# Kernel tuning notes

Measured on AMD Instinct MI355X. Metric: run time of the kernel, lower is better.

## Reference

```python
import jax, jax.numpy as jnp
import numpy as np

TOTAL = 131072   # total frames across all utterances
SEG = 256        # number of utterances
FEAT = 78        # input feature dim (hardcoded by Linear(78,1024))
HID = 1024
NCLS = 10


def _linear_params(key, fan_in, fan_out):
    # torch nn.Linear default init: U(-1/sqrt(fan_in), 1/sqrt(fan_in))
    bound = 1.0 / np.sqrt(fan_in)
    kw, kb = jax.random.split(key)
    W = jax.random.uniform(kw, (fan_in, fan_out), minval=-bound, maxval=bound, dtype=jnp.float32)
    b = jax.random.uniform(kb, (fan_out,), minval=-bound, maxval=bound, dtype=jnp.float32)
    return W, b


def setup_inputs() -> dict:
    key = jax.random.key(0)
    ks = jax.random.split(key, 8)
    # ragged lengths summing exactly to TOTAL
    rng = np.random.default_rng(0)
    raw = rng.integers(256, 768, size=SEG).astype(np.float64)
    lens = np.maximum(1, (raw * TOTAL / raw.sum()).astype(np.int64))
    lens[-1] += TOTAL - lens.sum()
    lengths = jnp.asarray(lens, dtype=jnp.int32)

    x = jax.random.normal(ks[0], (TOTAL, FEAT), dtype=jnp.float32)
    W1, b1 = _linear_params(ks[1], FEAT, HID)
    W2, b2 = _linear_params(ks[2], HID, HID)
    W3, b3 = _linear_params(ks[3], HID, HID)
    W4, b4 = _linear_params(ks[4], HID, HID)
    W5, b5 = _linear_params(ks[5], HID, 1)
    W6, b6 = _linear_params(ks[6], HID, HID)
    W7, b7 = _linear_params(ks[7], HID, NCLS)
    return dict(x=x, W1=W1, b1=b1, W2=W2, b2=b2, W3=W3, b3=b3, W4=W4, b4=b4,
                W5=W5, b5=b5, W6=W6, b6=b6, W7=W7, b7=b7, lengths=lengths)


def reference(x, W1, b1, W2, b2, W3, b3, W4, b4, W5, b5, W6, b6, W7, b7, lengths):
    h = jax.nn.relu(x @ W1 + b1)
    h = jax.nn.relu(h @ W2 + b2)
    h = jax.nn.relu(h @ W3 + b3)
    h = jax.nn.relu(h @ W4 + b4)            # [N, HID]
    scores = jax.nn.relu(h @ W5 + b5)[:, 0]  # per-frame attention logit [N]

    # per-segment softmax over frames, then weighted sum pooling (fused segment ops)
    n_seg = lengths.shape[0]
    seg = jnp.repeat(jnp.arange(n_seg, dtype=jnp.int32), lengths,
                     total_repeat_length=h.shape[0])          # [N] segment ids
    m = jax.ops.segment_max(scores, seg, num_segments=n_seg)  # stable softmax max
    e = jnp.exp(scores - m[seg])
    denom = jax.ops.segment_sum(e, seg, num_segments=n_seg)
    w = e / denom[seg]                                        # [N] softmax weights
    pooled = jax.ops.segment_sum(h * w[:, None], seg, num_segments=n_seg)  # [SEG, HID]

    out = jax.nn.relu(pooled @ W6 + b6) @ W7 + b7             # [SEG, 10]
    return out
```

## Files before the change

### kernel.cpp

```cpp
#include <hip/hip_runtime.h>
#include <hip/hip_fp16.h>

#define TOTAL 131072
#define SEGN  256
#define FEAT  78
#define FPAD  96
#define HID   1024
#define NCLS  10
#define FCHUNK 32

typedef __attribute__((ext_vector_type(8))) short short8;
typedef __attribute__((ext_vector_type(4))) float floatx4;

typedef __attribute__((address_space(1))) void gvoid_t;
typedef __attribute__((address_space(3))) void svoid_t;

__device__ __forceinline__ void async_copy16(const void* gsrc, void* ldst) {
    __builtin_amdgcn_global_load_lds((gvoid_t*)(void*)gsrc, (svoid_t*)ldst, 16, 0, 0);
}


__global__ void conv_x_slab(const float* __restrict__ x, __half* __restrict__ xb,
                            int row0, int rows) {
    int idx = blockIdx.x * 256 + threadIdx.x;
    if (idx >= rows * FPAD) return;
    int col = idx % FPAD;
    int r   = idx / FPAD;
    float v = (col < FEAT) ? x[(size_t)(row0 + r) * FEAT + col] : 0.0f;
    xb[idx] = __float2half(v);
}

__global__ void conv_wt_kernel(const float* __restrict__ W, __half* __restrict__ Wt,
                               int K, int N, int Kpad) {
    int idx = blockIdx.x * 256 + threadIdx.x;
    if (idx >= N * Kpad) return;
    int k = idx % Kpad;
    int n = idx / Kpad;
    float v = (k < K) ? W[(size_t)k * N + n] : 0.0f;
    Wt[idx] = __float2half(v);
}

__global__ void conv_w4_kernel(const float* __restrict__ W2, const float* __restrict__ W3,
                               const float* __restrict__ W4, const float* __restrict__ W6,
                               __half* __restrict__ w2t, __half* __restrict__ w3t,
                               __half* __restrict__ w4t, __half* __restrict__ w6t) {
    int idx = blockIdx.x * 256 + threadIdx.x;
    if (idx >= HID * HID) return;
    int k = idx % HID;
    int n = idx / HID;
    const float* Ws[4] = {W2, W3, W4, W6};
    __half* Ts[4] = {w2t, w3t, w4t, w6t};
    int w = blockIdx.y;
    Ts[w][idx] = __float2half(Ws[w][(size_t)k * HID + n]);
}


#define VMCNT(n)  asm volatile("s_waitcnt vmcnt(" #n ")" ::: "memory")
#define SBAR      __builtin_amdgcn_s_barrier()

#define STAGE_A(TT) do { short* d_ = smem + (((TT)&3)<<14); \
    async_copy16(gA + (TT)*32, d_ + t*8); \
    async_copy16(gA + (TT)*32 + kstr128, d_ + 4096 + t*8); } while (0)
#define STAGE_B(TT) do { short* d_ = smem + (((TT)&3)<<14) + 8192; \
    async_copy16(gB + (TT)*32, d_ + t*8); \
    async_copy16(gB + (TT)*32 + kstr128, d_ + 4096 + t*8); } while (0)

#define TILE_BODY(TT, DO_STAGE, VM) do { \
    const short* base_ = smem + (((TT)&3)<<14); \
    short8 af0_[4], af1_[4], bf_[4]; \
    _Pragma("unroll") \
    for (int i_ = 0; i_ < 4; ++i_) af0_[i_] = *(const short8*)&base_[aoff + i_*512]; \
    _Pragma("unroll") \
    for (int i_ = 0; i_ < 4; ++i_) bf_[i_]  = *(const short8*)&base_[8192 + boff + i_*512]; \
    _Pragma("unroll") \
    for (int i_ = 0; i_ < 4; ++i_) af1_[i_] = *(const short8*)&base_[2048 + aoff + i_*512]; \
    if (DO_STAGE) { STAGE_A((TT)+3); STAGE_B((TT)+3); } \
    __builtin_amdgcn_s_setprio(1); \
    _Pragma("unroll") \
    for (int mi_ = 0; mi_ < 4; ++mi_) \
        _Pragma("unroll") \
        for (int ni_ = 0; ni_ < 4; ++ni_) \
            acc[mi_][ni_] = __builtin_amdgcn_mfma_f32_16x16x32_f16( \
                af0_[mi_], bf_[ni_], acc[mi_][ni_], 0, 0, 0); \
    _Pragma("unroll") \
    for (int mi_ = 0; mi_ < 4; ++mi_) \
        _Pragma("unroll") \
        for (int ni_ = 0; ni_ < 4; ++ni_) \
            acc[4+mi_][ni_] = __builtin_amdgcn_mfma_f32_16x16x32_f16( \
                af1_[mi_], bf_[ni_], acc[4+mi_][ni_], 0, 0, 0); \
    __builtin_amdgcn_s_setprio(0); \
    VM; \
    SBAR; \
} while (0)

__global__ __launch_bounds__(512, 2)
void gemm256(const __half* __restrict__ A, const __half* __restrict__ Bt,
             __half* __restrict__ C, const float* __restrict__ bias,
             int M, int N, int K, int relu_flag,
             const float* __restrict__ W5g, float* __restrict__ scores_p)
{
    __shared__ __align__(16) short smem[4 * 16384];

    const int t   = threadIdx.x;
    const int nbn = N >> 8;
    const int nbm = M >> 8;
    int bm, bn;
    {
        const int b = blockIdx.x;
        if ((nbm & 7) == 0) {
            const int xcd = b & 7;
            const int j   = b >> 3;
            bm = xcd * (nbm >> 3) + j / nbn;
            bn = j % nbn;
        } else {
            bn = b % nbn;
            bm = b / nbn;
        }
    }
    const size_t m0 = (size_t)bm << 8;
    const size_t n0 = (size_t)bn << 8;
    const int wave = t >> 6, lane = t & 63;
    const int wmb = (wave >> 2) << 7;
    const int wnb = (wave & 3) << 6;
    const int l16 = lane & 15, q = lane >> 4;
    const int qa  = q ^ ((l16 >> 1) & 3);
    const int aoff = (wmb + l16) * 32 + qa * 8;
    const int boff = (wnb + l16) * 32 + qa * 8;

    const int rr = t >> 2;
    const int qs = ((t & 3) ^ ((t >> 3) & 3)) * 8;
    const __half* gA = A  + (m0 + rr) * K + qs;
    const __half* gB = Bt + (n0 + rr) * K + qs;
    const int kstr128 = K << 7;

    floatx4 acc[8][4] = {};
    const int NT = K >> 5;

    STAGE_A(0); STAGE_B(0);
    STAGE_A(1); STAGE_B(1);
    STAGE_A(2); STAGE_B(2);
    VMCNT(4);
    SBAR;

    int T = 0;
    for (; T < NT - 3; ++T)
        TILE_BODY(T, 1, VMCNT(4));
    TILE_BODY(T, 0, VMCNT(0)); ++T;
    TILE_BODY(T, 0, (void)0);  ++T;
    TILE_BODY(T, 0, (void)0);
    __syncthreads();

    __half* ct = (__half*)smem;
#pragma unroll
    for (int ni = 0; ni < 4; ++ni) {
        const int col = wnb + ni * 16 + l16;
        const float bv = bias[n0 + col];
#pragma unroll
        for (int mi = 0; mi < 8; ++mi) {
            const int r0l = wmb + mi * 16 + q * 4;
#pragma unroll
            for (int r = 0; r < 4; ++r) {
                float v = acc[mi][ni][r] + bv;
                if (relu_flag) v = fmaxf(v, 0.0f);
                ct[(r0l + r) * 256 + col] = __float2half(v);
            }
        }
    }
    __syncthreads();
#pragma unroll
    for (int it = 0; it < 16; ++it) {
        const int chunk = it * 512 + t;
        const int row = chunk >> 5;
        const int c32 = chunk & 31;
        short8 v = *(const short8*)&ct[row * 256 + c32 * 8];
        *(short8*)&C[(m0 + row) * N + n0 + c32 * 8] = v;
        if (scores_p) {
            const float* wv = W5g + n0 + c32 * 8;
            float p = 0.f;
#pragma unroll
            for (int j = 0; j < 8; ++j)
                p += __half2float(((const __half*)&v)[j]) * wv[j];
#pragma unroll
            for (int o = 16; o > 0; o >>= 1) p += __shfl_down(p, o, 32);
            if ((t & 31) == 0)
                scores_p[(size_t)bn * M + m0 + row] = p;
        }
    }
}


__global__ __launch_bounds__(256, 2)
void gemm_f16(const __half* __restrict__ A, const __half* __restrict__ Bt,
              __half* __restrict__ C, const float* __restrict__ bias,
              int M, int N, int K, int relu_flag,
              const float* __restrict__ W5g, float* __restrict__ scores_p)
{
    __shared__ __align__(16) short smem[4 * 128 * 32];
    short* lds_a0 = smem;
    short* lds_a1 = smem + 128 * 32;
    short* lds_b0 = smem + 2 * 128 * 32;
    short* lds_b1 = smem + 3 * 128 * 32;

    const int t   = threadIdx.x;
    const int nbn = N >> 7;
    const int nbm = M >> 7;
    int bm, bn;
    {
        const int b = blockIdx.x;
        if ((nbm & 7) == 0) {
            const int xcd = b & 7;
            const int j   = b >> 3;
            bm = xcd * (nbm >> 3) + j / nbn;
            bn = j % nbn;
        } else {
            bn = b % nbn;
            bm = b / nbn;
        }
    }
    const size_t m0 = (size_t)bm * 128;
    const size_t n0 = (size_t)bn * 128;
    const int wave = t >> 6, lane = t & 63;
    const int wm = (wave >> 1) << 6;
    const int wn = (wave & 1) << 6;
    const int l16 = lane & 15, q = lane >> 4;

    floatx4 acc[4][4] = {};

    const int c0 = t, c1 = t + 256;
    const __half* a0 = A  + (m0 + (size_t)(c0 >> 2)) * K + (c0 & 3) * 8;
    const __half* a1 = A  + (m0 + (size_t)(c1 >> 2)) * K + (c1 & 3) * 8;
    const __half* b0 = Bt + (n0 + (size_t)(c0 >> 2)) * K + (c0 & 3) * 8;
    const __half* b1 = Bt + (n0 + (size_t)(c1 >> 2)) * K + (c1 & 3) * 8;
    short* lA0_0 = &lds_a0[c0 * 8];
    short* lA0_1 = &lds_a0[c1 * 8];
    short* lA1_0 = &lds_a1[c0 * 8];
    short* lA1_1 = &lds_a1[c1 * 8];
    short* lB0_0 = &lds_b0[c0 * 8];
    short* lB0_1 = &lds_b0[c1 * 8];
    short* lB1_0 = &lds_b1[c0 * 8];
    short* lB1_1 = &lds_b1[c1 * 8];

    for (int k0 = 0; k0 < K; k0 += 64) {
        __syncthreads();
        async_copy16(a0 + k0, lA0_0);
        async_copy16(a1 + k0, lA0_1);
        async_copy16(b0 + k0, lB0_0);
        async_copy16(b1 + k0, lB0_1);
        async_copy16(a0 + k0 + 32, lA1_0);
        async_copy16(a1 + k0 + 32, lA1_1);
        async_copy16(b0 + k0 + 32, lB1_0);
        async_copy16(b1 + k0 + 32, lB1_1);
        __syncthreads();

        short8 af[4], bfv[4];
#pragma unroll
        for (int i = 0; i < 4; ++i)
            af[i] = *(const short8*)&lds_a0[(wm + i * 16 + l16) * 32 + q * 8];
#pragma unroll
        for (int i = 0; i < 4; ++i)
            bfv[i] = *(const short8*)&lds_b0[(wn + i * 16 + l16) * 32 + q * 8];
#pragma unroll
        for (int mi = 0; mi < 4; ++mi)
#pragma unroll
            for (int ni = 0; ni < 4; ++ni)
                acc[mi][ni] = __builtin_amdgcn_mfma_f32_16x16x32_f16(
                    af[mi], bfv[ni], acc[mi][ni], 0, 0, 0);

#pragma unroll
        for (int i = 0; i < 4; ++i)
            af[i] = *(const short8*)&lds_a1[(wm + i * 16 + l16) * 32 + q * 8];
#pragma unroll
        for (int i = 0; i < 4; ++i)
            bfv[i] = *(const short8*)&lds_b1[(wn + i * 16 + l16) * 32 + q * 8];
#pragma unroll
        for (int mi = 0; mi < 4; ++mi)
#pragma unroll
            for (int ni = 0; ni < 4; ++ni)
                acc[mi][ni] = __builtin_amdgcn_mfma_f32_16x16x32_f16(
                    af[mi], bfv[ni], acc[mi][ni], 0, 0, 0);
    }

    __half* ct = (__half*)smem;
#pragma unroll
    for (int h = 0; h < 2; ++h) {
        __syncthreads();
        if (wm == h * 64) {
#pragma unroll
            for (int ni = 0; ni < 4; ++ni) {
                const int col = wn + ni * 16 + l16;
                const float bv = bias[n0 + col];
#pragma unroll
                for (int mi = 0; mi < 4; ++mi) {
                    const int r0l = mi * 16 + q * 4;
#pragma unroll
                    for (int r = 0; r < 4; ++r) {
                        float v = acc[mi][ni][r] + bv;
                        if (relu_flag) v = fmaxf(v, 0.0f);
                        ct[(r0l + r) * 128 + col] = __float2half(v);
                    }
                }
            }
        }
        __syncthreads();
#pragma unroll
        for (int it = 0; it < 4; ++it) {
            const int chunk = it * 256 + t;
            const int row = chunk >> 4;
            const int off = (chunk & 15) * 8;
            short8 v = *(const short8*)&ct[row * 128 + off];
            *(short8*)&C[(m0 + h * 64 + row) * N + n0 + off] = v;
            if (scores_p) {
                const float* wv = W5g + n0 + off;
                float p = 0.f;
#pragma unroll
                for (int j = 0; j < 8; ++j)
                    p += __half2float(((const __half*)&v)[j]) * wv[j];
#pragma unroll
                for (int o = 8; o > 0; o >>= 1) p += __shfl_down(p, o, 16);
                if (l16 == 0)
                    scores_p[(size_t)bn * M + m0 + h * 64 + row] = p;
            }
        }
    }
}


__global__ __launch_bounds__(256, 2)
void gemm_k96(const __half* __restrict__ A, const __half* __restrict__ Bt,
              __half* __restrict__ C, const float* __restrict__ bias, int M, int N)
{
    __shared__ __align__(16) short smem[2 * 128 * 96];
    short* lds_a = smem;
    short* lds_b = smem + 128 * 96;

    const int t   = threadIdx.x;
    const int nbn = N >> 7;
    const int nbm = M >> 7;
    int bm, bn;
    {
        const int b = blockIdx.x;
        if ((nbm & 7) == 0) {
            const int xcd = b & 7;
            const int j   = b >> 3;
            bm = xcd * (nbm >> 3) + j / nbn;
            bn = j % nbn;
        } else {
            bn = b % nbn;
            bm = b / nbn;
        }
    }
    const size_t m0 = (size_t)bm * 128;
    const size_t n0 = (size_t)bn * 128;
    const int wave = t >> 6, lane = t & 63;
    const int wm = (wave >> 1) << 6;
    const int wn = (wave & 1) << 6;
    const int l16 = lane & 15, q = lane >> 4;

#pragma unroll
    for (int i = 0; i < 6; ++i) {
        const int c = i * 256 + t;
        const int r = c / 12, j = c % 12;
        async_copy16(A  + (m0 + (size_t)r) * 96 + j * 8, &lds_a[c * 8]);
        async_copy16(Bt + (n0 + (size_t)r) * 96 + j * 8, &lds_b[c * 8]);
    }
    __syncthreads();

    floatx4 acc[4][4] = {};
#pragma unroll
    for (int ks = 0; ks < 3; ++ks) {
        short8 af[4], bfv[4];
        const int xo = ks * 32 + q * 8;
#pragma unroll
        for (int i = 0; i < 4; ++i)
            af[i] = *(const short8*)&lds_a[(wm + i * 16 + l16) * 96 + xo];
#pragma unroll
        for (int i = 0; i < 4; ++i)
            bfv[i] = *(const short8*)&lds_b[(wn + i * 16 + l16) * 96 + xo];
#pragma unroll
        for (int mi = 0; mi < 4; ++mi)
#pragma unroll
            for (int ni = 0; ni < 4; ++ni)
                acc[mi][ni] = __builtin_amdgcn_mfma_f32_16x16x32_f16(
                    af[mi], bfv[ni], acc[mi][ni], 0, 0, 0);
    }

    __half* ct = (__half*)smem;
#pragma unroll
    for (int h = 0; h < 2; ++h) {
        __syncthreads();
        if (wm == h * 64) {
#pragma unroll
            for (int ni = 0; ni < 4; ++ni) {
                const int col = wn + ni * 16 + l16;
                const float bv = bias[n0 + col];
#pragma unroll
                for (int mi = 0; mi < 4; ++mi) {
                    const int r0l = mi * 16 + q * 4;
#pragma unroll
                    for (int r = 0; r < 4; ++r) {
                        float v = fmaxf(acc[mi][ni][r] + bv, 0.0f);
                        ct[(r0l + r) * 128 + col] = __float2half(v);
                    }
                }
            }
        }
        __syncthreads();
#pragma unroll
        for (int it = 0; it < 4; ++it) {
            const int chunk = it * 256 + t;
            const int row = chunk >> 4;
            const int off = (chunk & 15) * 8;
            *(short8*)&C[(m0 + h * 64 + row) * N + n0 + off] =
                *(const short8*)&ct[row * 128 + off];
        }
    }
}


__global__ void seg_offsets_kernel(const int* __restrict__ lengths, int* __restrict__ off) {
    if (blockIdx.x == 0 && threadIdx.x == 0) {
        int a = 0;
        off[0] = 0;
        for (int i = 0; i < SEGN; ++i) { a += lengths[i]; off[i + 1] = a; }
    }
}


__global__ __launch_bounds__(256)
void scorepool_kernel(const __half* __restrict__ h4, int slab_beg, int slab_rows,
                      const float* __restrict__ scores_p, const float* __restrict__ b5,
                      const int* __restrict__ segoff,
                      float* __restrict__ pooled, float* __restrict__ denom)
{
    __shared__ float e_sh[FCHUNK];
    const int t = threadIdx.x;
    const int f0 = slab_beg + blockIdx.x * FCHUNK;

    if (t < FCHUNK) {
        const int fl = f0 - slab_beg + t;
        float sc = 0.f;
#pragma unroll
        for (int b = 0; b < 4; ++b) sc += scores_p[(size_t)b * slab_rows + fl];
        sc = fmaxf(sc + b5[0], 0.0f);
        e_sh[t] = __expf(fminf(sc, 80.0f));
    }
    __syncthreads();

    const int c0 = t * 4;
    int lo = 0, hi = SEGN - 1;
    while (lo < hi) {
        int mid = (lo + hi + 1) >> 1;
        if (segoff[mid] <= f0) lo = mid; else hi = mid - 1;
    }
    int s = lo;
    int f = f0;
    const int fend = f0 + FCHUNK;
    const __half* base = h4 + (size_t)(f0 - slab_beg) * HID + c0;
    while (f < fend) {
        int send = segoff[s + 1];
        if (send > fend) send = fend;
        float a0 = 0.f, a1 = 0.f, a2 = 0.f, a3 = 0.f, es = 0.f;
        for (; f < send; ++f, base += HID) {
            float e = e_sh[f - f0];
            const __half2* r2 = (const __half2*)base;
            float2 u = __half22float2(r2[0]);
            float2 v = __half22float2(r2[1]);
            a0 += e * u.x; a1 += e * u.y; a2 += e * v.x; a3 += e * v.y;
            es += e;
        }
        float* p = pooled + (size_t)s * HID + c0;
        atomicAdd(p,     a0);
        atomicAdd(p + 1, a1);
        atomicAdd(p + 2, a2);
        atomicAdd(p + 3, a3);
        if (t == 0) atomicAdd(&denom[s], es);
        ++s;
    }
}


__global__ __launch_bounds__(256)
void finalize_pool_kernel(const float* __restrict__ pooled, const float* __restrict__ denom,
                          __half* __restrict__ poolh)
{
    int s = blockIdx.x, t = threadIdx.x;
    float inv = 1.0f / denom[s];
    for (int j = t; j < HID; j += 256)
        poolh[(size_t)s * HID + j] = __float2half(pooled[(size_t)s * HID + j] * inv);
}


__global__ void final_kernel(const __half* __restrict__ z, const float* __restrict__ W7,
                             const float* __restrict__ b7, float* __restrict__ out) {
    int s = blockIdx.x, t = threadIdx.x;
    float loc[NCLS];
#pragma unroll
    for (int c = 0; c < NCLS; ++c) loc[c] = 0.f;
    for (int k = t; k < HID; k += 256) {
        float zk = __half2float(z[(size_t)s * HID + k]);
        const float* wr = W7 + k * NCLS;
#pragma unroll
        for (int c = 0; c < NCLS; ++c) loc[c] += zk * wr[c];
    }
#pragma unroll
    for (int c = 0; c < NCLS; ++c)
#pragma unroll
        for (int o = 32; o > 0; o >>= 1) loc[c] += __shfl_down(loc[c], o);
    __shared__ float accs[NCLS];
    if (t < NCLS) accs[t] = 0.f;
    __syncthreads();
    if ((t & 63) == 0)
        for (int c = 0; c < NCLS; ++c) atomicAdd(&accs[c], loc[c]);
    __syncthreads();
    if (t < NCLS) out[s * NCLS + t] = accs[t] + b7[t];
}


extern "C" void kernel_launch(void* const* d_in, const int* in_sizes, int n_in,
                              void* d_out, int out_size, void* d_ws, size_t ws_size,
                              hipStream_t stream) {
    const float* x  = (const float*)d_in[0];
    const float* W1 = (const float*)d_in[1];
    const float* b1 = (const float*)d_in[2];
    const float* W2 = (const float*)d_in[3];
    const float* b2 = (const float*)d_in[4];
    const float* W3 = (const float*)d_in[5];
    const float* b3 = (const float*)d_in[6];
    const float* W4 = (const float*)d_in[7];
    const float* b4 = (const float*)d_in[8];
    const float* W5 = (const float*)d_in[9];
    const float* b5 = (const float*)d_in[10];
    const float* W6 = (const float*)d_in[11];
    const float* b6 = (const float*)d_in[12];
    const float* W7 = (const float*)d_in[13];
    const float* b7 = (const float*)d_in[14];
    const int* lengths = (const int*)d_in[15];
    float* out = (float*)d_out;

    char* ws = (char*)d_ws;
    size_t off = 0;
    auto take = [&](size_t bytes) -> char* {
        char* p = ws + off;
        off = (off + bytes + 255) & ~(size_t)255;
        return p;
    };
    __half* w1t   = (__half*)take((size_t)HID * FPAD * 2);
    __half* w2t   = (__half*)take((size_t)HID * HID * 2);
    __half* w3t   = (__half*)take((size_t)HID * HID * 2);
    __half* w4t   = (__half*)take((size_t)HID * HID * 2);
    __half* w6t   = (__half*)take((size_t)HID * HID * 2);
    int*    segoff = (int*)take((SEGN + 1) * 4);
    float*  pooled = (float*)take((size_t)SEGN * HID * 4);
    float*  denom  = (float*)take(SEGN * 4);
    __half* poolh  = (__half*)take((size_t)SEGN * HID * 2);
    __half* z      = (__half*)take((size_t)SEGN * HID * 2);

    int R = TOTAL;
    while (R > 1024) {
        size_t need = off + (size_t)R * FPAD * 2 + 2 * (size_t)R * HID * 2
                    + (size_t)8 * R * 4 + 4 * 256;
        if (need <= ws_size) break;
        R >>= 1;
    }
    __half* slabX    = (__half*)take((size_t)R * FPAD * 2);
    __half* slabA    = (__half*)take((size_t)R * HID * 2);
    __half* slabB    = (__half*)take((size_t)R * HID * 2);
    float*  scores_p = (float*)take((size_t)8 * R * 4);

    seg_offsets_kernel<<<1, 64, 0, stream>>>(lengths, segoff);
    hipMemsetAsync(pooled, 0, (size_t)SEGN * HID * 4, stream);
    hipMemsetAsync(denom, 0, SEGN * 4, stream);

    conv_wt_kernel<<<(HID * FPAD + 255) / 256, 256, 0, stream>>>(W1, w1t, FEAT, HID, FPAD);
    dim3 gW((HID * HID + 255) / 256, 4);
    conv_w4_kernel<<<gW, 256, 0, stream>>>(W2, W3, W4, W6, w2t, w3t, w4t, w6t);

    const int nBlocksSlab = (R / 128) * (HID / 128);
    const int nBlocks256  = (R / 256) * (HID / 256);
    for (int sb = 0; sb < TOTAL; sb += R) {
        conv_x_slab<<<(R * FPAD + 255) / 256, 256, 0, stream>>>(x, slabX, sb, R);
        gemm_k96<<<nBlocksSlab, 256, 0, stream>>>(slabX, w1t, slabA, b1, R, HID);
        gemm256<<<nBlocks256, 512, 0, stream>>>(slabA, w2t, slabB, b2, R, HID, HID, 1,
                                                nullptr, nullptr);
        gemm256<<<nBlocks256, 512, 0, stream>>>(slabB, w3t, slabA, b3, R, HID, HID, 1,
                                                nullptr, nullptr);
        gemm256<<<nBlocks256, 512, 0, stream>>>(slabA, w4t, slabB, b4, R, HID, HID, 1,
                                                W5, scores_p);
        scorepool_kernel<<<R / FCHUNK, 256, 0, stream>>>(slabB, sb, R, scores_p, b5,
                                                         segoff, pooled, denom);
    }

    finalize_pool_kernel<<<SEGN, 256, 0, stream>>>(pooled, denom, poolh);
    const int nBlocksHead = (SEGN / 128) * (HID / 128);
    gemm_f16<<<nBlocksHead, 256, 0, stream>>>(poolh, w6t, z, b6, SEGN, HID, HID, 1,
                                              nullptr, nullptr);
    final_kernel<<<SEGN, 256, 0, stream>>>(z, W7, b7, out);
}
```

Measured before the change: 1.240 ms.

## Fuse x fp32-to-fp16 conversion into first GEMM and retune scorepool blocking

Removes the separate conv_x_slab kernel and its padded half-precision slab. The first-layer GEMM now reads fp32 x directly, converts it to half, and writes it into LDS, saving a launch and a global round trip. The scorepool kernel now uses 512 threads with 2 columns each and 128-frame chunks, which cuts the number of blocks and atomics per column. Merging the staging macros is only a cosmetic change. Tradeoffs: the GEMM's A load becomes a synchronous strided read rather than an async copy, and the unaligned float2 reads of 78-wide rows may reduce efficiency.

```diff
diff --git a/kernel.cpp b/kernel.cpp
--- a/kernel.cpp
+++ b/kernel.cpp
@@ -7,7 +7,7 @@
 #define FPAD  96
 #define HID   1024
 #define NCLS  10
-#define FCHUNK 32
+#define FCHUNK 128
 
 typedef __attribute__((ext_vector_type(8))) short short8;
 typedef __attribute__((ext_vector_type(4))) float floatx4;
@@ -19,16 +19,6 @@
     __builtin_amdgcn_global_load_lds((gvoid_t*)(void*)gsrc, (svoid_t*)ldst, 16, 0, 0);
 }
 
-
-__global__ void conv_x_slab(const float* __restrict__ x, __half* __restrict__ xb,
-                            int row0, int rows) {
-    int idx = blockIdx.x * 256 + threadIdx.x;
-    if (idx >= rows * FPAD) return;
-    int col = idx % FPAD;
-    int r   = idx / FPAD;
-    float v = (col < FEAT) ? x[(size_t)(row0 + r) * FEAT + col] : 0.0f;
-    xb[idx] = __float2half(v);
-}
 
 __global__ void conv_wt_kernel(const float* __restrict__ W, __half* __restrict__ Wt,
                                int K, int N, int Kpad) {
@@ -58,12 +48,11 @@
 #define VMCNT(n)  asm volatile("s_waitcnt vmcnt(" #n ")" ::: "memory")
 #define SBAR      __builtin_amdgcn_s_barrier()
 
-#define STAGE_A(TT) do { short* d_ = smem + (((TT)&3)<<14); \
-    async_copy16(gA + (TT)*32, d_ + t*8); \
-    async_copy16(gA + (TT)*32 + kstr128, d_ + 4096 + t*8); } while (0)
-#define STAGE_B(TT) do { short* d_ = smem + (((TT)&3)<<14) + 8192; \
-    async_copy16(gB + (TT)*32, d_ + t*8); \
-    async_copy16(gB + (TT)*32 + kstr128, d_ + 4096 + t*8); } while (0)
+#define STAGE(TT) do { short* d_ = smem + (((TT)&3)<<14); \
+    async_copy16(gA + (TT)*32,           d_ + t*8); \
+    async_copy16(gA + (TT)*32 + kstr128, d_ + 4096 + t*8); \
+    async_copy16(gB + (TT)*32,           d_ + 8192 + t*8); \
+    async_copy16(gB + (TT)*32 + kstr128, d_ + 12288 + t*8); } while (0)
 
 #define TILE_BODY(TT, DO_STAGE, VM) do { \
     const short* base_ = smem + (((TT)&3)<<14); \
@@ -74,7 +63,7 @@
     for (int i_ = 0; i_ < 4; ++i_) bf_[i_]  = *(const short8*)&base_[8192 + boff + i_*512]; \
     _Pragma("unroll") \
     for (int i_ = 0; i_ < 4; ++i_) af1_[i_] = *(const short8*)&base_[2048 + aoff + i_*512]; \
-    if (DO_STAGE) { STAGE_A((TT)+3); STAGE_B((TT)+3); } \
+    if (DO_STAGE) STAGE((TT)+3); \
     __builtin_amdgcn_s_setprio(1); \
     _Pragma("unroll") \
     for (int mi_ = 0; mi_ < 4; ++mi_) \
@@ -136,9 +125,7 @@
     floatx4 acc[8][4] = {};
     const int NT = K >> 5;
 
-    STAGE_A(0); STAGE_B(0);
-    STAGE_A(1); STAGE_B(1);
-    STAGE_A(2); STAGE_B(2);
+    STAGE(0); STAGE(1); STAGE(2);
     VMCNT(4);
     SBAR;
 
@@ -326,8 +313,9 @@
 
 
 __global__ __launch_bounds__(256, 2)
-void gemm_k96(const __half* __restrict__ A, const __half* __restrict__ Bt,
-              __half* __restrict__ C, const float* __restrict__ bias, int M, int N)
+void gemm_k96(const float* __restrict__ X, const __half* __restrict__ Bt,
+              __half* __restrict__ C, const float* __restrict__ bias,
+              int M, int N, int row0)
 {
     __shared__ __align__(16) short smem[2 * 128 * 96];
     short* lds_a = smem;
@@ -360,8 +348,18 @@
     for (int i = 0; i < 6; ++i) {
         const int c = i * 256 + t;
         const int r = c / 12, j = c % 12;
-        async_copy16(A  + (m0 + (size_t)r) * 96 + j * 8, &lds_a[c * 8]);
         async_copy16(Bt + (n0 + (size_t)r) * 96 + j * 8, &lds_b[c * 8]);
+    }
+
+#pragma unroll
+    for (int i = 0; i < 24; ++i) {
+        const int idx = i * 256 + t;
+        const int row = idx / 48;
+        const int c2  = idx % 48;
+        float2 v = make_float2(0.f, 0.f);
+        if (c2 < 39)
+            v = *(const float2*)&X[(size_t)(row0 + m0 + row) * FEAT + c2 * 2];
+        *(__half2*)&lds_a[row * 96 + c2 * 2] = __float22half2_rn(v);
     }
     __syncthreads();
 
@@ -426,7 +424,7 @@
 }
 
 
-__global__ __launch_bounds__(256)
+__global__ __launch_bounds__(512)
 void scorepool_kernel(const __half* __restrict__ h4, int slab_beg, int slab_rows,
                       const float* __restrict__ scores_p, const float* __restrict__ b5,
                       const int* __restrict__ segoff,
@@ -446,7 +444,7 @@
     }
     __syncthreads();
 
-    const int c0 = t * 4;
+    const int c0 = t * 2;
     int lo = 0, hi = SEGN - 1;
     while (lo < hi) {
         int mid = (lo + hi + 1) >> 1;
@@ -459,20 +457,16 @@
     while (f < fend) {
         int send = segoff[s + 1];
         if (send > fend) send = fend;
-        float a0 = 0.f, a1 = 0.f, a2 = 0.f, a3 = 0.f, es = 0.f;
+        float a0 = 0.f, a1 = 0.f, es = 0.f;
         for (; f < send; ++f, base += HID) {
             float e = e_sh[f - f0];
-            const __half2* r2 = (const __half2*)base;
-            float2 u = __half22float2(r2[0]);
-            float2 v = __half22float2(r2[1]);
-            a0 += e * u.x; a1 += e * u.y; a2 += e * v.x; a3 += e * v.y;
+            float2 u = __half22float2(*(const __half2*)base);
+            a0 += e * u.x; a1 += e * u.y;
             es += e;
         }
         float* p = pooled + (size_t)s * HID + c0;
         atomicAdd(p,     a0);
         atomicAdd(p + 1, a1);
-        atomicAdd(p + 2, a2);
-        atomicAdd(p + 3, a3);
         if (t == 0) atomicAdd(&denom[s], es);
         ++s;
     }
@@ -557,12 +551,10 @@
 
     int R = TOTAL;
     while (R > 1024) {
-        size_t need = off + (size_t)R * FPAD * 2 + 2 * (size_t)R * HID * 2
-                    + (size_t)8 * R * 4 + 4 * 256;
+        size_t need = off + 2 * (size_t)R * HID * 2 + (size_t)8 * R * 4 + 4 * 256;
         if (need <= ws_size) break;
         R >>= 1;
     }
-    __half* slabX    = (__half*)take((size_t)R * FPAD * 2);
     __half* slabA    = (__half*)take((size_t)R * HID * 2);
     __half* slabB    = (__half*)take((size_t)R * HID * 2);
     float*  scores_p = (float*)take((size_t)8 * R * 4);
@@ -578,15 +570,14 @@
     const int nBlocksSlab = (R / 128) * (HID / 128);
     const int nBlocks256  = (R / 256) * (HID / 256);
     for (int sb = 0; sb < TOTAL; sb += R) {
-        conv_x_slab<<<(R * FPAD + 255) / 256, 256, 0, stream>>>(x, slabX, sb, R);
-        gemm_k96<<<nBlocksSlab, 256, 0, stream>>>(slabX, w1t, slabA, b1, R, HID);
+        gemm_k96<<<nBlocksSlab, 256, 0, stream>>>(x, w1t, slabA, b1, R, HID, sb);
         gemm256<<<nBlocks256, 512, 0, stream>>>(slabA, w2t, slabB, b2, R, HID, HID, 1,
                                                 nullptr, nullptr);
         gemm256<<<nBlocks256, 512, 0, stream>>>(slabB, w3t, slabA, b3, R, HID, HID, 1,
                                                 nullptr, nullptr);
         gemm256<<<nBlocks256, 512, 0, stream>>>(slabA, w4t, slabB, b4, R, HID, HID, 1,
                                                 W5, scores_p);
-        scorepool_kernel<<<R / FCHUNK, 256, 0, stream>>>(slabB, sb, R, scores_p, b5,
+        scorepool_kernel<<<R / FCHUNK, 512, 0, stream>>>(slabB, sb, R, scores_p, b5,
                                                          segoff, pooled, denom);
     }
 
```

New measurement: 1.396 ms. 12.5% more time.
